# Optimization experiments

Hardware: AMD Instinct MI355X
Metric: run time of the kernel (lower is better)

## Reference

```python
import jax, jax.numpy as jnp
import numpy as np

H, W = 48, 48
L = H * W            # 2304 tokens
D = 256              # d_model
NH = 8               # heads (self and memory attn)
FF = 1024            # dim_feedforward
T = 2                # memory frames
BS = 1
GN_GROUPS = 32       # GNActDWConv2d default groups


def layernorm(x, g, b, eps=1e-5):
    m = jnp.mean(x, -1, keepdims=True)
    v = jnp.mean((x - m) ** 2, -1, keepdims=True)
    return (x - m) * jax.lax.rsqrt(v + eps) * g + b


def linear(x, Wt, b):
    # torch nn.Linear convention: Wt is [out, in]
    return x @ Wt.T + b


def mha_core(Q, K, V, nhead):
    # Q [Lq, bs, C], K/V [Lk, bs, C]; AOT MultiheadAttention core (eval: no dropout)
    Lq, bs, C = Q.shape
    hd = C // nhead
    Qh = (Q / np.float32(np.sqrt(hd))).reshape(Lq, bs, nhead, hd).transpose(1, 2, 0, 3)
    Kh = K.reshape(-1, bs, nhead, hd).transpose(1, 2, 0, 3)
    Vh = V.reshape(-1, bs, nhead, hd).transpose(1, 2, 0, 3)
    attn = jax.nn.softmax(jnp.einsum('bhqd,bhkd->bhqk', Qh, Kh), axis=-1)
    out = jnp.einsum('bhqk,bhkd->bhqd', attn, Vh)
    return out.transpose(2, 0, 1, 3).reshape(Lq, bs, C)


def groupnorm(x, g, b, groups, eps=1e-5):
    bs, c, h, w = x.shape
    xg = x.reshape(bs, groups, c // groups, h, w)
    m = jnp.mean(xg, (2, 3, 4), keepdims=True)
    v = jnp.mean((xg - m) ** 2, (2, 3, 4), keepdims=True)
    xg = (xg - m) * jax.lax.rsqrt(v + eps)
    return xg.reshape(bs, c, h, w) * g[None, :, None, None] + b[None, :, None, None]


def dwconv5(x, k):
    # depthwise 5x5, padding=2; x [bs,c,h,w], k [c,1,5,5]
    return jax.lax.conv_general_dilated(x, k, (1, 1), ((2, 2), (2, 2)),
                                        feature_group_count=x.shape[1])


def setup_inputs() -> dict:
    key = jax.random.key(0)
    ks = jax.random.split(key, 16)
    rn = lambda i, shape, s=1.0: jax.random.normal(ks[i], shape, jnp.float32) * s
    w = 0.02
    inp = {
        'tgt': rn(0, (L, BS, D)),
        'global_K': rn(1, (T, L, BS, D)),
        'global_V': rn(2, (T, L, BS, D)),
        'local_K': rn(3, (L, BS, D)),
        'local_V': rn(4, (L, BS, D)),
        # LayerNorms
        'ln1_g': jnp.ones(D, jnp.float32), 'ln1_b': jnp.zeros(D, jnp.float32),
        'ln2_g': jnp.ones(D, jnp.float32), 'ln2_b': jnp.zeros(D, jnp.float32),
        'ln3_g': jnp.ones(D, jnp.float32), 'ln3_b': jnp.zeros(D, jnp.float32),
        'ln4_g': jnp.ones(D, jnp.float32), 'ln4_b': jnp.zeros(D, jnp.float32),
        # self_attn (use_linear=True) Q/K/V + projection
        'sa_Wq': rn(5, (D, D), w), 'sa_bq': jnp.zeros(D, jnp.float32),
        'sa_Wk': rn(6, (D, D), w), 'sa_bk': jnp.zeros(D, jnp.float32),
        'sa_Wv': rn(7, (D, D), w), 'sa_bv': jnp.zeros(D, jnp.float32),
        'sa_Wo': rn(8, (D, D), w), 'sa_bo': jnp.zeros(D, jnp.float32),
        # block linear_Q
        'Wq': rn(9, (D, D), w), 'bq': jnp.zeros(D, jnp.float32),
        # long/short term attn projections (use_linear=False)
        'lt_Wo': rn(10, (D, D), w), 'lt_bo': jnp.zeros(D, jnp.float32),
        'st_Wo': rn(11, (D, D), w), 'st_bo': jnp.zeros(D, jnp.float32),
        # FFN: linear1 -> GN+GELU+DWConv -> linear2
        'W1': rn(12, (FF, D), w), 'b1': jnp.zeros(FF, jnp.float32),
        'gn_g': jnp.ones(FF, jnp.float32), 'gn_b': jnp.zeros(FF, jnp.float32),
        'dw_k': rn(13, (FF, 1, 5, 5), 0.05),
        'W2': rn(14, (D, FF), w), 'b2': jnp.zeros(D, jnp.float32),
    }
    return inp


def reference(tgt, global_K, global_V, local_K, local_V,
              ln1_g, ln1_b, ln2_g, ln2_b, ln3_g, ln3_b, ln4_g, ln4_b,
              sa_Wq, sa_bq, sa_Wk, sa_bk, sa_Wv, sa_bv, sa_Wo, sa_bo,
              Wq, bq, lt_Wo, lt_bo, st_Wo, st_bo,
              W1, b1, gn_g, gn_b, dw_k, W2, b2):
    # --- stage 1: self-attention ---
    _tgt = layernorm(tgt, ln1_g, ln1_b)
    q = linear(_tgt, sa_Wq, sa_bq)
    k = linear(_tgt, sa_Wk, sa_bk)
    v = linear(_tgt, sa_Wv, sa_bv)
    tgt2 = linear(mha_core(q, k, v, NH), sa_Wo, sa_bo)
    tgt = tgt + tgt2  # droppath is identity at eval

    # --- stage 2: long-term + short-term memory cross-attention ---
    _tgt = layernorm(tgt, ln2_g, ln2_b)
    curr_Q = linear(_tgt, Wq, bq)
    curr_K = curr_Q
    curr_V = _tgt

    flat_K = global_K.reshape(-1, BS, D)  # [T*L, bs, D]
    flat_V = global_V.reshape(-1, BS, D)
    tgt2 = linear(mha_core(curr_Q, flat_K, flat_V, NH), lt_Wo, lt_bo)

    k_st = layernorm(local_K + curr_K, ln4_g, ln4_b)
    v_st = layernorm(local_V + curr_V, ln4_g, ln4_b)
    tgt3 = linear(mha_core(curr_Q, k_st, v_st, NH), st_Wo, st_bo)

    tgt = tgt + tgt2 + tgt3

    # --- stage 3: FFN with GN + GELU + depthwise conv ---
    _tgt = layernorm(tgt, ln3_g, ln3_b)
    x = linear(_tgt, W1, b1)                        # [L, bs, FF]
    x = x.reshape(H, W, BS, FF).transpose(2, 3, 0, 1)  # [bs, FF, H, W]
    x = jax.nn.gelu(groupnorm(x, gn_g, gn_b, GN_GROUPS), approximate=False)
    x = dwconv5(x, dw_k)
    x = x.reshape(BS, FF, L).transpose(2, 0, 1)     # [L, bs, FF]
    tgt2 = linear(x, W2, b2)
    return tgt + tgt2
```

## Files before the change

kernel.cpp:

```cpp
#include <hip/hip_runtime.h>
#include <hip/hip_bf16.h>

#define L   2304
#define D   256
#define NHD 8
#define HD  32
#define FF  1024
#define HH  48
#define WWW 48
#define SPL 4
#define RCH 24
#define RP  (L / RCH)
#define S2LOG 0.25503486f

typedef unsigned short bfraw;
typedef __attribute__((ext_vector_type(8))) short s8v;
typedef __attribute__((ext_vector_type(4))) float f4v;

__device__ __forceinline__ bfraw f2b(float x) {
    __hip_bfloat16 h = __float2bfloat16(x);
    return __builtin_bit_cast(bfraw, h);
}

__global__ __launch_bounds__(256) void diag_kernel(float* __restrict__ out, float c, int n)
{
    int i = blockIdx.x * 256 + threadIdx.x;
    if (i < n) out[i] = c;
}

__global__ __launch_bounds__(256) void ln_kernel(
    const float* __restrict__ inA, const float* __restrict__ inB,
    const float* __restrict__ g, const float* __restrict__ b,
    float* __restrict__ out, bfraw* __restrict__ outb)
{
    int row = blockIdx.x, t = threadIdx.x;
    size_t idx = (size_t)row * D + t;
    float v = inA[idx];
    if (inB) v += inB[idx];
    __shared__ float rs[256], rq[256];
    rs[t] = v; rq[t] = v * v;
    __syncthreads();
    for (int o = 128; o > 0; o >>= 1) {
        if (t < o) { rs[t] += rs[t + o]; rq[t] += rq[t + o]; }
        __syncthreads();
    }
    float mean = rs[0] * (1.f / D);
    float var  = rq[0] * (1.f / D) - mean * mean;
    float rstd = rsqrtf(var + 1e-5f);
    float r = (v - mean) * rstd * g[t] + b[t];
    if (out)  out[idx]  = r;
    if (outb) outb[idx] = f2b(r);
}

__global__ __launch_bounds__(256) void ln2_ln4v(
    const float* __restrict__ t5, const float* __restrict__ lV,
    const float* __restrict__ g2, const float* __restrict__ b2,
    const float* __restrict__ g4, const float* __restrict__ b4,
    bfraw* __restrict__ out2b, float* __restrict__ outv)
{
    int row = blockIdx.x, t = threadIdx.x;
    size_t idx = (size_t)row * D + t;
    float v = t5[idx];
    __shared__ float rs[256], rq[256];
    rs[t] = v; rq[t] = v * v;
    __syncthreads();
    for (int o = 128; o > 0; o >>= 1) {
        if (t < o) { rs[t] += rs[t + o]; rq[t] += rq[t + o]; }
        __syncthreads();
    }
    float mean = rs[0] * (1.f / D);
    float var  = rq[0] * (1.f / D) - mean * mean;
    float rstd = rsqrtf(var + 1e-5f);
    float r2 = (v - mean) * rstd * g2[t] + b2[t];
    out2b[idx] = f2b(r2);
    float u = r2 + lV[idx];
    __syncthreads();
    rs[t] = u; rq[t] = u * u;
    __syncthreads();
    for (int o = 128; o > 0; o >>= 1) {
        if (t < o) { rs[t] += rs[t + o]; rq[t] += rq[t + o]; }
        __syncthreads();
    }
    float mean2 = rs[0] * (1.f / D);
    float var2  = rq[0] * (1.f / D) - mean2 * mean2;
    float rstd2 = rsqrtf(var2 + 1e-5f);
    outv[idx] = (u - mean2) * rstd2 * g4[t] + b4[t];
}

__global__ __launch_bounds__(256) void ln_cvtT(
    const float* __restrict__ t1, const float* __restrict__ lK,
    const float* __restrict__ g4, const float* __restrict__ b4,
    bfraw* __restrict__ kb2,
    const float* __restrict__ vsrc, bfraw* __restrict__ vtb2)
{
    __shared__ float rs[256], rq[256];
    __shared__ float Ls[32][33];
    int t = threadIdx.x;
    if (blockIdx.x < L) {
        int row = blockIdx.x;
        size_t idx = (size_t)row * D + t;
        float v = t1[idx] + lK[idx];
        rs[t] = v; rq[t] = v * v;
        __syncthreads();
        for (int o = 128; o > 0; o >>= 1) {
            if (t < o) { rs[t] += rs[t + o]; rq[t] += rq[t + o]; }
            __syncthreads();
        }
        float mean = rs[0] * (1.f / D);
        float var  = rq[0] * (1.f / D) - mean * mean;
        float rstd = rsqrtf(var + 1e-5f);
        kb2[idx] = f2b((v - mean) * rstd * g4[t] + b4[t]);
    } else {
        int idx = blockIdx.x - L;
        int n0 = (idx >> 3) * 32, h = idx & 7;
        int nl = t >> 3, dq = t & 7;
        float4 v = *reinterpret_cast<const float4*>(vsrc + (size_t)(n0 + nl) * D + h * HD + dq * 4);
        Ls[nl][dq*4+0] = v.x; Ls[nl][dq*4+1] = v.y;
        Ls[nl][dq*4+2] = v.z; Ls[nl][dq*4+3] = v.w;
        __syncthreads();
        int dl = t >> 3, nq = t & 7;
        ushort4 o;
        o.x = f2b(Ls[nq*4+0][dl]); o.y = f2b(Ls[nq*4+1][dl]);
        o.z = f2b(Ls[nq*4+2][dl]); o.w = f2b(Ls[nq*4+3][dl]);
        *reinterpret_cast<ushort4*>(vtb2 + (size_t)(h * HD + dl) * L + n0 + nq * 4) = o;
    }
}

__global__ __launch_bounds__(256) void gemm_mfma(
    const bfraw* __restrict__ A, const float* __restrict__ W,
    const float* __restrict__ bias, const float* res, float* out,
    bfraw* __restrict__ outb, float oscale,
    int M, int N, int K)
{
    __shared__ __attribute__((aligned(16))) short Wl[64][32];
    int t = threadIdx.x;
    int w = t >> 6, l = t & 63;
    int lo = l & 15, quad = l >> 4;
    int m0 = blockIdx.x * 32, n0 = blockIdx.y * 64;
    int wr = (w & 1) * 16, wc = (w >> 1) * 32;
    f4v acc[2];
    acc[0] = (f4v){0.f, 0.f, 0.f, 0.f};
    acc[1] = (f4v){0.f, 0.f, 0.f, 0.f};

    int aswz = (quad ^ ((lo >> 2) & 3)) * 8;
    int srow = t >> 3, spart = t & 7;
    const bfraw* ap = A + (size_t)(m0 + wr + lo) * K + quad * 8;

    for (int k0 = 0; k0 < K; k0 += 32) {
        float4 w4[2];
        #pragma unroll
        for (int i = 0; i < 2; i++)
            w4[i] = *reinterpret_cast<const float4*>(W + (size_t)(n0 + i * 32 + srow) * K + k0 + spart * 4);
        s8v af = *reinterpret_cast<const s8v*>(ap + k0);
        __syncthreads();
        #pragma unroll
        for (int i = 0; i < 2; i++) {
            int row = i * 32 + srow;
            int col = ((spart >> 1) ^ ((row >> 2) & 3)) * 8 + (spart & 1) * 4;
            ushort4 wb;
            wb.x = f2b(w4[i].x); wb.y = f2b(w4[i].y); wb.z = f2b(w4[i].z); wb.w = f2b(w4[i].w);
            *reinterpret_cast<ushort4*>(&Wl[row][col]) = wb;
        }
        __syncthreads();
        #pragma unroll
        for (int j = 0; j < 2; j++) {
            int rw = wc + j * 16 + lo;
            s8v wf = *reinterpret_cast<const s8v*>(&Wl[rw][aswz]);
            acc[j] = __builtin_amdgcn_mfma_f32_16x16x32_bf16(af, wf, acc[j], 0, 0, 0);
        }
    }

    #pragma unroll
    for (int j = 0; j < 2; j++) {
        #pragma unroll
        for (int r = 0; r < 4; r++) {
            int mrow = m0 + wr + quad * 4 + r;
            int ncol = n0 + wc + j * 16 + lo;
            float v = acc[j][r] + bias[ncol];
            size_t idx = (size_t)mrow * N + ncol;
            if (res) v += res[idx];
            if (out) out[idx] = v;
            if (outb) outb[idx] = f2b(v * oscale);
        }
    }
}

__global__ __launch_bounds__(256) void gemm_dual(
    const bfraw* __restrict__ A1, const float* __restrict__ W1, const float* __restrict__ b1,
    const bfraw* __restrict__ A2, const float* __restrict__ W2, const float* __restrict__ b2,
    const float* __restrict__ res, float* __restrict__ out)
{
    __shared__ __attribute__((aligned(16))) short Wl[64][32];
    int t = threadIdx.x;
    int w = t >> 6, l = t & 63;
    int lo = l & 15, quad = l >> 4;
    int m0 = blockIdx.x * 32, n0 = blockIdx.y * 64;
    int wr = (w & 1) * 16, wc = (w >> 1) * 32;
    f4v acc[2];
    acc[0] = (f4v){0.f, 0.f, 0.f, 0.f};
    acc[1] = (f4v){0.f, 0.f, 0.f, 0.f};

    int aswz = (quad ^ ((lo >> 2) & 3)) * 8;
    int srow = t >> 3, spart = t & 7;

    #pragma unroll
    for (int half = 0; half < 2; half++) {
        const bfraw* ap = (half ? A2 : A1) + (size_t)(m0 + wr + lo) * D + quad * 8;
        const float* W  = half ? W2 : W1;
        for (int k0 = 0; k0 < D; k0 += 32) {
            float4 w4[2];
            #pragma unroll
            for (int i = 0; i < 2; i++)
                w4[i] = *reinterpret_cast<const float4*>(W + (size_t)(n0 + i * 32 + srow) * D + k0 + spart * 4);
            s8v af = *reinterpret_cast<const s8v*>(ap + k0);
            __syncthreads();
            #pragma unroll
            for (int i = 0; i < 2; i++) {
                int row = i * 32 + srow;
                int col = ((spart >> 1) ^ ((row >> 2) & 3)) * 8 + (spart & 1) * 4;
                ushort4 wb;
                wb.x = f2b(w4[i].x); wb.y = f2b(w4[i].y); wb.z = f2b(w4[i].z); wb.w = f2b(w4[i].w);
                *reinterpret_cast<ushort4*>(&Wl[row][col]) = wb;
            }
            __syncthreads();
            #pragma unroll
            for (int j = 0; j < 2; j++) {
                int rw = wc + j * 16 + lo;
                s8v wf = *reinterpret_cast<const s8v*>(&Wl[rw][aswz]);
                acc[j] = __builtin_amdgcn_mfma_f32_16x16x32_bf16(af, wf, acc[j], 0, 0, 0);
            }
        }
    }

    #pragma unroll
    for (int j = 0; j < 2; j++) {
        #pragma unroll
        for (int r = 0; r < 4; r++) {
            int mrow = m0 + wr + quad * 4 + r;
            int ncol = n0 + wc + j * 16 + lo;
            size_t idx = (size_t)mrow * D + ncol;
            out[idx] = acc[j][r] + b1[ncol] + b2[ncol] + res[idx];
        }
    }
}

__global__ __launch_bounds__(256) void gemm_qkv(
    const bfraw* __restrict__ A,
    const float* __restrict__ Wq_, const float* __restrict__ bq_,
    const float* __restrict__ Wk_, const float* __restrict__ bk_,
    const float* __restrict__ Wv_, const float* __restrict__ bv_,
    bfraw* __restrict__ qb, bfraw* __restrict__ kb, bfraw* __restrict__ vtb)
{
    __shared__ __attribute__((aligned(16))) short Wl[64][32];
    int t = threadIdx.x;
    int w = t >> 6, l = t & 63;
    int lo = l & 15, quad = l >> 4;
    int sel = blockIdx.y >> 2;
    int m0 = blockIdx.x * 32, n0 = (blockIdx.y & 3) * 64;
    int wr = (w & 1) * 16, wc = (w >> 1) * 32;
    const float* W    = (sel == 0) ? Wq_ : (sel == 1) ? Wk_ : Wv_;
    const float* bias = (sel == 0) ? bq_ : (sel == 1) ? bk_ : bv_;
    f4v acc[2];
    acc[0] = (f4v){0.f, 0.f, 0.f, 0.f};
    acc[1] = (f4v){0.f, 0.f, 0.f, 0.f};

    int aswz = (quad ^ ((lo >> 2) & 3)) * 8;
    int srow = t >> 3, spart = t & 7;
    const bfraw* ap = A + (size_t)(m0 + wr + lo) * D + quad * 8;

    for (int k0 = 0; k0 < D; k0 += 32) {
        float4 w4[2];
        #pragma unroll
        for (int i = 0; i < 2; i++)
            w4[i] = *reinterpret_cast<const float4*>(W + (size_t)(n0 + i * 32 + srow) * D + k0 + spart * 4);
        s8v af = *reinterpret_cast<const s8v*>(ap + k0);
        __syncthreads();
        #pragma unroll
        for (int i = 0; i < 2; i++) {
            int row = i * 32 + srow;
            int col = ((spart >> 1) ^ ((row >> 2) & 3)) * 8 + (spart & 1) * 4;
            ushort4 wb;
            wb.x = f2b(w4[i].x); wb.y = f2b(w4[i].y); wb.z = f2b(w4[i].z); wb.w = f2b(w4[i].w);
            *reinterpret_cast<ushort4*>(&Wl[row][col]) = wb;
        }
        __syncthreads();
        #pragma unroll
        for (int j = 0; j < 2; j++) {
            int rw = wc + j * 16 + lo;
            s8v wf = *reinterpret_cast<const s8v*>(&Wl[rw][aswz]);
            acc[j] = __builtin_amdgcn_mfma_f32_16x16x32_bf16(af, wf, acc[j], 0, 0, 0);
        }
    }

    #pragma unroll
    for (int j = 0; j < 2; j++) {
        #pragma unroll
        for (int r = 0; r < 4; r++) {
            int mrow = m0 + wr + quad * 4 + r;
            int ncol = n0 + wc + j * 16 + lo;
            float v = acc[j][r] + bias[ncol];
            if (sel == 0)      qb[(size_t)mrow * D + ncol] = f2b(v * S2LOG);
            else if (sel == 1) kb[(size_t)mrow * D + ncol] = f2b(v);
            else               vtb[(size_t)ncol * L + mrow] = f2b(v);
        }
    }
}

__global__ __launch_bounds__(256) void cvt_both(
    const float* __restrict__ gK, bfraw* __restrict__ kb1,
    const float* __restrict__ gV, bfraw* __restrict__ vtb1)
{
    __shared__ float Ls[32][33];
    int t = threadIdx.x;
    if (blockIdx.y < NHD) {
        int h = blockIdx.y, n0 = blockIdx.x * 32;
        const int N = 2 * L;
        int nl = t >> 3, dq = t & 7;
        float4 v = *reinterpret_cast<const float4*>(gV + (size_t)(n0 + nl) * D + h * HD + dq * 4);
        Ls[nl][dq*4+0] = v.x; Ls[nl][dq*4+1] = v.y;
        Ls[nl][dq*4+2] = v.z; Ls[nl][dq*4+3] = v.w;
        __syncthreads();
        int dl = t >> 3, nq = t & 7;
        ushort4 o;
        o.x = f2b(Ls[nq*4+0][dl]); o.y = f2b(Ls[nq*4+1][dl]);
        o.z = f2b(Ls[nq*4+2][dl]); o.w = f2b(Ls[nq*4+3][dl]);
        *reinterpret_cast<ushort4*>(vtb1 + (size_t)(h * HD + dl) * N + n0 + nq * 4) = o;
    } else {
        size_t i = ((size_t)(blockIdx.x * 8 + (blockIdx.y - NHD)) * 256 + t) * 4;
        float4 v = *reinterpret_cast<const float4*>(gK + i);
        ushort4 o;
        o.x = f2b(v.x); o.y = f2b(v.y); o.z = f2b(v.z); o.w = f2b(v.w);
        *reinterpret_cast<ushort4*>(kb1 + i) = o;
    }
}

__device__ __forceinline__ void attn_core(
    const bfraw* __restrict__ Qb, const bfraw* __restrict__ Kb,
    const bfraw* __restrict__ Vt, float* __restrict__ OP,
    float* __restrict__ ML, int Lk, int chunk, int zz,
    short (*Ks)[32], short (*Vts)[72], short (*Ps)[72], float (*Tb)[33])
{
    int t = threadIdx.x;
    int w = t >> 6, l = t & 63;
    int h = blockIdx.y, q0 = blockIdx.x * 64 + w * 16;
    int lo = l & 15, quad = l >> 4;
    int kb = zz * chunk, ke = kb + chunk;

    s8v qf = *reinterpret_cast<const s8v*>(Qb + (size_t)(q0 + lo) * D + h * HD + quad * 8);
    int kswz = (quad ^ ((lo >> 2) & 3)) * 8;

    int skey = t >> 2, spart = t & 3;
    int kcol = (spart ^ ((skey >> 2) & 3)) * 8;
    int sd = t >> 3, svp = t & 7;
    const bfraw* kp = Kb + (size_t)skey * D + h * HD + spart * 8;
    const bfraw* vp = Vt + (size_t)(h * HD + sd) * Lk + svp * 8;

    float l_r = 0.f;
    f4v o0 = {0.f, 0.f, 0.f, 0.f}, o1 = {0.f, 0.f, 0.f, 0.f};

    for (int k0 = kb; k0 < ke; k0 += 64) {
        s8v kv = *reinterpret_cast<const s8v*>(kp + (size_t)k0 * D);
        s8v vv = *reinterpret_cast<const s8v*>(vp + k0);
        __syncthreads();
        *reinterpret_cast<s8v*>(&Ks[skey][kcol]) = kv;
        *reinterpret_cast<s8v*>(&Vts[sd][svp * 8]) = vv;
        __syncthreads();

        f4v sc4[4];
        #pragma unroll
        for (int s = 0; s < 4; s++) {
            s8v kf = *reinterpret_cast<const s8v*>(&Ks[lo + 16 * s][kswz]);
            sc4[s] = __builtin_amdgcn_mfma_f32_16x16x32_bf16(kf, qf, (f4v){0.f,0.f,0.f,0.f}, 0, 0, 0);
        }
        float ls = 0.f;
        #pragma unroll
        for (int s = 0; s < 4; s++) {
            float p0 = __builtin_amdgcn_exp2f(sc4[s][0]);
            float p1 = __builtin_amdgcn_exp2f(sc4[s][1]);
            float p2 = __builtin_amdgcn_exp2f(sc4[s][2]);
            float p3 = __builtin_amdgcn_exp2f(sc4[s][3]);
            ls += p0 + p1 + p2 + p3;
            ushort4 pk;
            pk.x = f2b(p0); pk.y = f2b(p1); pk.z = f2b(p2); pk.w = f2b(p3);
            *reinterpret_cast<ushort4*>(&Ps[lo][s * 16 + quad * 4]) = pk;
        }
        ls += __shfl_xor(ls, 16);
        ls += __shfl_xor(ls, 32);
        l_r += ls;
        #pragma unroll
        for (int kc = 0; kc < 2; kc++) {
            s8v pf = *reinterpret_cast<const s8v*>(&Ps[lo][kc * 32 + quad * 8]);
            s8v v0 = *reinterpret_cast<const s8v*>(&Vts[lo][kc * 32 + quad * 8]);
            s8v v1 = *reinterpret_cast<const s8v*>(&Vts[16 + lo][kc * 32 + quad * 8]);
            o0 = __builtin_amdgcn_mfma_f32_16x16x32_bf16(v0, pf, o0, 0, 0, 0);
            o1 = __builtin_amdgcn_mfma_f32_16x16x32_bf16(v1, pf, o1, 0, 0, 0);
        }
    }

    #pragma unroll
    for (int r = 0; r < 4; r++) {
        Tb[lo][quad * 4 + r]      = o0[r];
        Tb[lo][16 + quad * 4 + r] = o1[r];
    }
    float* Oz = OP + (size_t)zz * L * D;
    int ql = l >> 2, dq = (l & 3) * 8;
    float4 u0, u1;
    u0.x = Tb[ql][dq + 0]; u0.y = Tb[ql][dq + 1];
    u0.z = Tb[ql][dq + 2]; u0.w = Tb[ql][dq + 3];
    u1.x = Tb[ql][dq + 4]; u1.y = Tb[ql][dq + 5];
    u1.z = Tb[ql][dq + 6]; u1.w = Tb[ql][dq + 7];
    *reinterpret_cast<float4*>(Oz + (size_t)(q0 + ql) * D + h * HD + dq)     = u0;
    *reinterpret_cast<float4*>(Oz + (size_t)(q0 + ql) * D + h * HD + dq + 4) = u1;
    if (l < 16)
        ML[((size_t)zz * NHD + h) * L + q0 + lo] = l_r;
}

__global__ __launch_bounds__(256) void attn_mfma_split(
    const bfraw* __restrict__ Qb, const bfraw* __restrict__ Kb,
    const bfraw* __restrict__ Vt, float* __restrict__ OP,
    float* __restrict__ ML, int Lk, int chunk)
{
    __shared__ __attribute__((aligned(16))) short Ks[64][32];
    __shared__ __attribute__((aligned(16))) short Vts[32][72];
    __shared__ __attribute__((aligned(16))) short Ps[4][16][72];
    __shared__ float Tb[4][16][33];
    int w = threadIdx.x >> 6;
    attn_core(Qb, Kb, Vt, OP, ML, Lk, chunk, blockIdx.z, Ks, Vts, Ps[w], Tb[w]);
}

__global__ __launch_bounds__(256) void attn_ltst(
    const bfraw* __restrict__ Qb,
    const bfraw* __restrict__ K_lt, const bfraw* __restrict__ V_lt,
    float* __restrict__ OP_lt, float* __restrict__ ML_lt,
    const bfraw* __restrict__ K_st, const bfraw* __restrict__ V_st,
    float* __restrict__ OP_st, float* __restrict__ ML_st)
{
    __shared__ __attribute__((aligned(16))) short Ks[64][32];
    __shared__ __attribute__((aligned(16))) short Vts[32][72];
    __shared__ __attribute__((aligned(16))) short Ps[4][16][72];
    __shared__ float Tb[4][16][33];
    int w = threadIdx.x >> 6;
    int z = blockIdx.z;
    if (z < 2)
        attn_core(Qb, K_lt, V_lt, OP_lt, ML_lt, 2 * L, L, z, Ks, Vts, Ps[w], Tb[w]);
    else
        attn_core(Qb, K_st, V_st, OP_st, ML_st, L, L / 2, z - 2, Ks, Vts, Ps[w], Tb[w]);
}

__global__ __launch_bounds__(256) void attn_combine(
    const float* __restrict__ OP, const float* __restrict__ ML,
    bfraw* __restrict__ Ob)
{
    int q = blockIdx.x, t = threadIdx.x, h = t >> 5;
    float wl = 0.f, acc = 0.f;
    #pragma unroll
    for (int s = 0; s < SPL; s++) {
        wl  += ML[((size_t)s * NHD + h) * L + q];
        acc += OP[(size_t)s * L * D + (size_t)q * D + t];
    }
    Ob[(size_t)q * D + t] = f2b(acc / wl);
}

__global__ __launch_bounds__(256) void combine2_both(
    const float* __restrict__ OP_lt, const float* __restrict__ ML_lt, bfraw* __restrict__ Ob_lt,
    const float* __restrict__ OP_st, const float* __restrict__ ML_st, bfraw* __restrict__ Ob_st)
{
    int q = blockIdx.x, t = threadIdx.x, h = t >> 5;
    const float* OP = blockIdx.y ? OP_st : OP_lt;
    const float* ML = blockIdx.y ? ML_st : ML_lt;
    bfraw* Ob = blockIdx.y ? Ob_st : Ob_lt;
    float wl = 0.f, acc = 0.f;
    #pragma unroll
    for (int s = 0; s < 2; s++) {
        wl  += ML[((size_t)s * NHD + h) * L + q];
        acc += OP[(size_t)s * L * D + (size_t)q * D + t];
    }
    Ob[(size_t)q * D + t] = f2b(acc / wl);
}

__global__ __launch_bounds__(256) void gn_stats_part(
    const float* __restrict__ X, float* __restrict__ ps)
{
    int g = blockIdx.x, rc = blockIdx.y, t = threadIdx.x;
    int cq = (t & 7) * 4;
    int rl = t >> 3;
    int r0 = rc * RP;
    float s = 0.f, sq = 0.f;
    #pragma unroll
    for (int p = 0; p < RP / 32; p++) {
        int l = r0 + p * 32 + rl;
        float4 v = *reinterpret_cast<const float4*>(X + (size_t)l * FF + g * 32 + cq);
        s  += v.x + v.y + v.z + v.w;
        sq += v.x*v.x + v.y*v.y + v.z*v.z + v.w*v.w;
    }
    __shared__ float rs[256], rq[256];
    rs[t] = s; rq[t] = sq;
    __syncthreads();
    for (int o = 128; o > 0; o >>= 1) {
        if (t < o) { rs[t] += rs[t + o]; rq[t] += rq[t + o]; }
        __syncthreads();
    }
    if (t == 0) {
        ps[(g * RCH + rc) * 2]     = rs[0];
        ps[(g * RCH + rc) * 2 + 1] = rq[0];
    }
}

__global__ __launch_bounds__(256) void gn_gelu_dwconv(
    const float* __restrict__ X, const float* __restrict__ ps,
    const float* __restrict__ gg, const float* __restrict__ gb,
    const float* __restrict__ Kw, bfraw* __restrict__ Y)
{
    __shared__ float tile[144][64];
    int h0 = blockIdx.x * 8, w0 = blockIdx.y * 8, c0 = blockIdx.z * 64;
    int t = threadIdx.x;
    int c = t & 63;
    int cg = (c0 + c) >> 5;
    float s = 0.f, sq = 0.f;
    #pragma unroll
    for (int i = 0; i < RCH; i++) {
        s  += ps[(cg * RCH + i) * 2];
        sq += ps[(cg * RCH + i) * 2 + 1];
    }
    float n = (float)(L * 32);
    float mu = s / n;
    float rs = rsqrtf(sq / n - mu * mu + 1e-5f);
    float ga = gg[c0 + c], be = gb[c0 + c];

    for (int i = t; i < 144 * 64; i += 256) {
        int sp = i >> 6;
        int hy = h0 + (sp / 12) - 2, wx = w0 + (sp % 12) - 2;
        float v = 0.f;
        if (hy >= 0 && hy < HH && wx >= 0 && wx < WWW) {
            float x = X[(size_t)(hy * WWW + wx) * FF + c0 + c];
            x = (x - mu) * rs * ga + be;
            v = 0.5f * x * (1.f + erff(x * 0.70710678118654752f));
        }
        tile[sp][c] = v;
    }
    float kw[25];
    #pragma unroll
    for (int i = 0; i < 25; i++) kw[i] = Kw[(size_t)(c0 + c) * 25 + i];
    __syncthreads();

    int sgrp = t >> 6;
    for (int sIdx = 0; sIdx < 16; sIdx++) {
        int sp = sgrp * 16 + sIdx;
        int oh = sp >> 3, ow = sp & 7;
        float acc = 0.f;
        #pragma unroll
        for (int ky = 0; ky < 5; ky++)
            #pragma unroll
            for (int kx = 0; kx < 5; kx++)
                acc += tile[(oh + ky) * 12 + ow + kx][c] * kw[ky * 5 + kx];
        Y[(size_t)((h0 + oh) * WWW + w0 + ow) * FF + c0 + c] = f2b(acc);
    }
}

extern "C" void kernel_launch(void* const* d_in, const int* in_sizes, int n_in,
                              void* d_out, int out_size, void* d_ws, size_t ws_size,
                              hipStream_t stream)
{
    (void)in_sizes;
    float* out = (float*)d_out;

    if (n_in != 34) {
        diag_kernel<<<(out_size + 255) / 256, 256, 0, stream>>>(out, 2000.f, out_size);
        return;
    }

    const float* tgt    = (const float*)d_in[0];
    const float* gK     = (const float*)d_in[1];
    const float* gV     = (const float*)d_in[2];
    const float* lK     = (const float*)d_in[3];
    const float* lV     = (const float*)d_in[4];
    const float* ln1_g  = (const float*)d_in[5];
    const float* ln1_b  = (const float*)d_in[6];
    const float* ln2_g  = (const float*)d_in[7];
    const float* ln2_b  = (const float*)d_in[8];
    const float* ln3_g  = (const float*)d_in[9];
    const float* ln3_b  = (const float*)d_in[10];
    const float* ln4_g  = (const float*)d_in[11];
    const float* ln4_b  = (const float*)d_in[12];
    const float* sa_Wq  = (const float*)d_in[13];
    const float* sa_bq  = (const float*)d_in[14];
    const float* sa_Wk  = (const float*)d_in[15];
    const float* sa_bk  = (const float*)d_in[16];
    const float* sa_Wv  = (const float*)d_in[17];
    const float* sa_bv  = (const float*)d_in[18];
    const float* sa_Wo  = (const float*)d_in[19];
    const float* sa_bo  = (const float*)d_in[20];
    const float* Wq     = (const float*)d_in[21];
    const float* bq     = (const float*)d_in[22];
    const float* lt_Wo  = (const float*)d_in[23];
    const float* lt_bo  = (const float*)d_in[24];
    const float* st_Wo  = (const float*)d_in[25];
    const float* st_bo  = (const float*)d_in[26];
    const float* W1w    = (const float*)d_in[27];
    const float* b1w    = (const float*)d_in[28];
    const float* gn_g   = (const float*)d_in[29];
    const float* gn_b   = (const float*)d_in[30];
    const float* dw_k   = (const float*)d_in[31];
    const float* W2w    = (const float*)d_in[32];
    const float* b2w    = (const float*)d_in[33];

    const size_t LD = (size_t)L * D;
    const size_t NEED = (6 * LD + (size_t)L * FF + 64) * 4;
    float* ws = (float*)d_ws;
    float* t0 = ws + 0 * LD;
    float* t1 = ws + 1 * LD;
    float* t2 = ws + 2 * LD;
    float* t3 = ws + 3 * LD;
    float* t4 = ws + 4 * LD;
    float* t5 = ws + 5 * LD;
    float* X1 = t0;
    float* X2 = ws + 6 * LD;
    bfraw* qb   = (bfraw*)X2;
    bfraw* kb1  = qb + LD;
    bfraw* vtb1 = qb + 3 * LD;
    bfraw* kb2  = qb + 5 * LD;
    bfraw* vtb2 = qb + 6 * LD;
    float* OP   = ws;
    float* OPlt = t0;
    float* OPst = t2;
    float* ML   = X2 + (7 * LD) / 2;
    float* MLlt = ML;
    float* MLst = ML + 2 * (size_t)NHD * L;
    float* PS   = ML;
    bfraw* t0b  = (bfraw*)t0;
    bfraw* t3b  = (bfraw*)t3;
    bfraw* t4b  = (bfraw*)t4;
    bfraw* obLT = t4b;
    bfraw* obST = t4b + LD;
    bfraw* X2b  = (bfraw*)X2;

    if (ws_size < NEED) {
        int wsMiB = (int)(ws_size >> 20); if (wsMiB > 63) wsMiB = 63;
        diag_kernel<<<(out_size + 255) / 256, 256, 0, stream>>>(out, 64.f + (float)wsMiB, out_size);
        return;
    }

    dim3 gDD(L / 32, D / 64);
    dim3 gDF(L / 32, FF / 64);
    dim3 gQKV(L / 32, 12);
    dim3 gATS(L / 64, NHD, SPL);
    dim3 gAT2(L / 64, NHD, 4);
    dim3 gCB(2 * L / 32, NHD + 8);
    dim3 gC2(L, 2);
    dim3 gGN(32, RCH);
    dim3 gDW(6, 6, 16);

    ln_kernel<<<L, 256, 0, stream>>>(tgt, nullptr, ln1_g, ln1_b, nullptr, t0b);
    gemm_qkv<<<gQKV, 256, 0, stream>>>(t0b, sa_Wq, sa_bq, sa_Wk, sa_bk, sa_Wv, sa_bv,
                                       qb, kb2, vtb2);
    attn_mfma_split<<<gATS, 256, 0, stream>>>(qb, kb2, vtb2, OP, ML, L, L / SPL);
    attn_combine<<<L, 256, 0, stream>>>(OP, ML, t4b);
    gemm_mfma<<<gDD, 256, 0, stream>>>(t4b, sa_Wo, sa_bo, tgt, t5, nullptr, 1.f, L, D, D);

    ln2_ln4v<<<L, 256, 0, stream>>>(t5, lV, ln2_g, ln2_b, ln4_g, ln4_b, t3b, t0);
    gemm_mfma<<<gDD, 256, 0, stream>>>(t3b, Wq, bq, nullptr, t1, qb, S2LOG, L, D, D);
    ln_cvtT<<<L + (L / 32) * NHD, 256, 0, stream>>>(t1, lK, ln4_g, ln4_b, kb2, t0, vtb2);
    cvt_both<<<gCB, 256, 0, stream>>>(gK, kb1, gV, vtb1);
    attn_ltst<<<gAT2, 256, 0, stream>>>(qb, kb1, vtb1, OPlt, MLlt, kb2, vtb2, OPst, MLst);
    combine2_both<<<gC2, 256, 0, stream>>>(OPlt, MLlt, obLT, OPst, MLst, obST);
    gemm_dual<<<gDD, 256, 0, stream>>>(obLT, lt_Wo, lt_bo, obST, st_Wo, st_bo, t5, t5);

    ln_kernel<<<L, 256, 0, stream>>>(t5, nullptr, ln3_g, ln3_b, nullptr, t4b);
    gemm_mfma<<<gDF, 256, 0, stream>>>(t4b, W1w, b1w, nullptr, X1, nullptr, 1.f, L, FF, D);
    gn_stats_part<<<gGN, 256, 0, stream>>>(X1, PS);
    gn_gelu_dwconv<<<gDW, 256, 0, stream>>>(X1, PS, gn_g, gn_b, dw_k, X2b);
    gemm_mfma<<<gDD, 256, 0, stream>>>(X2b, W2w, b2w, t5, out, nullptr, 1.f, L, D, FF);
}
```

Measured before the change: 311.5 us.

## Fuse GN stats into W1 GEMM epilogue and merge memory cvt into LN2

Removes the separate GroupNorm partial-stats kernel: the FFN W1 GEMM epilogue now reduces per-wave sums and sums of squares via shuffles and atomically accumulates them per group into PS, which the LN3 kernel zeroes beforehand. The global K/V bf16 conversion kernel is merged into the LN2/LN4v kernel as extra blocks. This cuts two launches and a full re-read of the FFN activation, at the cost of float atomics (non-deterministic summation order) and an extra epilogue reduction in every GEMM call.

```diff
diff --git a/kernel.cpp b/kernel.cpp
--- a/kernel.cpp
+++ b/kernel.cpp
@@ -9,8 +9,6 @@
 #define HH  48
 #define WWW 48
 #define SPL 4
-#define RCH 24
-#define RP  (L / RCH)
 #define S2LOG 0.25503486f
 
 typedef unsigned short bfraw;
@@ -31,9 +29,11 @@
 __global__ __launch_bounds__(256) void ln_kernel(
     const float* __restrict__ inA, const float* __restrict__ inB,
     const float* __restrict__ g, const float* __restrict__ b,
-    float* __restrict__ out, bfraw* __restrict__ outb)
+    float* __restrict__ out, bfraw* __restrict__ outb,
+    float* __restrict__ zps)
 {
     int row = blockIdx.x, t = threadIdx.x;
+    if (zps && row == 0 && t < 64) zps[t] = 0.f;
     size_t idx = (size_t)row * D + t;
     float v = inA[idx];
     if (inB) v += inB[idx];
@@ -52,39 +52,68 @@
     if (outb) outb[idx] = f2b(r);
 }
 
-__global__ __launch_bounds__(256) void ln2_ln4v(
+__global__ __launch_bounds__(256) void ln2cvt(
     const float* __restrict__ t5, const float* __restrict__ lV,
     const float* __restrict__ g2, const float* __restrict__ b2,
     const float* __restrict__ g4, const float* __restrict__ b4,
-    bfraw* __restrict__ out2b, float* __restrict__ outv)
-{
-    int row = blockIdx.x, t = threadIdx.x;
-    size_t idx = (size_t)row * D + t;
-    float v = t5[idx];
+    bfraw* __restrict__ out2b, float* __restrict__ outv,
+    const float* __restrict__ gK, bfraw* __restrict__ kb1,
+    const float* __restrict__ gV, bfraw* __restrict__ vtb1)
+{
     __shared__ float rs[256], rq[256];
-    rs[t] = v; rq[t] = v * v;
-    __syncthreads();
-    for (int o = 128; o > 0; o >>= 1) {
-        if (t < o) { rs[t] += rs[t + o]; rq[t] += rq[t + o]; }
-        __syncthreads();
-    }
-    float mean = rs[0] * (1.f / D);
-    float var  = rq[0] * (1.f / D) - mean * mean;
-    float rstd = rsqrtf(var + 1e-5f);
-    float r2 = (v - mean) * rstd * g2[t] + b2[t];
-    out2b[idx] = f2b(r2);
-    float u = r2 + lV[idx];
-    __syncthreads();
-    rs[t] = u; rq[t] = u * u;
-    __syncthreads();
-    for (int o = 128; o > 0; o >>= 1) {
-        if (t < o) { rs[t] += rs[t + o]; rq[t] += rq[t + o]; }
-        __syncthreads();
-    }
-    float mean2 = rs[0] * (1.f / D);
-    float var2  = rq[0] * (1.f / D) - mean2 * mean2;
-    float rstd2 = rsqrtf(var2 + 1e-5f);
-    outv[idx] = (u - mean2) * rstd2 * g4[t] + b4[t];
+    __shared__ float Ls[32][33];
+    int t = threadIdx.x;
+    if (blockIdx.x < L) {
+        int row = blockIdx.x;
+        size_t idx = (size_t)row * D + t;
+        float v = t5[idx];
+        rs[t] = v; rq[t] = v * v;
+        __syncthreads();
+        for (int o = 128; o > 0; o >>= 1) {
+            if (t < o) { rs[t] += rs[t + o]; rq[t] += rq[t + o]; }
+            __syncthreads();
+        }
+        float mean = rs[0] * (1.f / D);
+        float var  = rq[0] * (1.f / D) - mean * mean;
+        float rstd = rsqrtf(var + 1e-5f);
+        float r2 = (v - mean) * rstd * g2[t] + b2[t];
+        out2b[idx] = f2b(r2);
+        float u = r2 + lV[idx];
+        __syncthreads();
+        rs[t] = u; rq[t] = u * u;
+        __syncthreads();
+        for (int o = 128; o > 0; o >>= 1) {
+            if (t < o) { rs[t] += rs[t + o]; rq[t] += rq[t + o]; }
+            __syncthreads();
+        }
+        float mean2 = rs[0] * (1.f / D);
+        float var2  = rq[0] * (1.f / D) - mean2 * mean2;
+        float rstd2 = rsqrtf(var2 + 1e-5f);
+        outv[idx] = (u - mean2) * rstd2 * g4[t] + b4[t];
+    } else {
+        int idx = blockIdx.x - L;
+        int ix = idx % (2 * L / 32), iy = idx / (2 * L / 32);
+        if (iy < NHD) {
+            int h = iy, n0 = ix * 32;
+            const int N = 2 * L;
+            int nl = t >> 3, dq = t & 7;
+            float4 v = *reinterpret_cast<const float4*>(gV + (size_t)(n0 + nl) * D + h * HD + dq * 4);
+            Ls[nl][dq*4+0] = v.x; Ls[nl][dq*4+1] = v.y;
+            Ls[nl][dq*4+2] = v.z; Ls[nl][dq*4+3] = v.w;
+            __syncthreads();
+            int dl = t >> 3, nq = t & 7;
+            ushort4 o;
+            o.x = f2b(Ls[nq*4+0][dl]); o.y = f2b(Ls[nq*4+1][dl]);
+            o.z = f2b(Ls[nq*4+2][dl]); o.w = f2b(Ls[nq*4+3][dl]);
+            *reinterpret_cast<ushort4*>(vtb1 + (size_t)(h * HD + dl) * N + n0 + nq * 4) = o;
+        } else {
+            size_t i = ((size_t)(ix * 8 + (iy - NHD)) * 256 + t) * 4;
+            float4 v = *reinterpret_cast<const float4*>(gK + i);
+            ushort4 o;
+            o.x = f2b(v.x); o.y = f2b(v.y); o.z = f2b(v.z); o.w = f2b(v.w);
+            *reinterpret_cast<ushort4*>(kb1 + i) = o;
+        }
+    }
 }
 
 __global__ __launch_bounds__(256) void ln_cvtT(
@@ -129,7 +158,7 @@
 __global__ __launch_bounds__(256) void gemm_mfma(
     const bfraw* __restrict__ A, const float* __restrict__ W,
     const float* __restrict__ bias, const float* res, float* out,
-    bfraw* __restrict__ outb, float oscale,
+    bfraw* __restrict__ outb, float oscale, float* __restrict__ ps,
     int M, int N, int K)
 {
     __shared__ __attribute__((aligned(16))) short Wl[64][32];
@@ -170,6 +199,7 @@
         }
     }
 
+    float sl = 0.f, sq = 0.f;
     #pragma unroll
     for (int j = 0; j < 2; j++) {
         #pragma unroll
@@ -181,6 +211,19 @@
             if (res) v += res[idx];
             if (out) out[idx] = v;
             if (outb) outb[idx] = f2b(v * oscale);
+            sl += v; sq += v * v;
+        }
+    }
+    if (ps) {
+        #pragma unroll
+        for (int off = 1; off < 64; off <<= 1) {
+            sl += __shfl_xor(sl, off);
+            sq += __shfl_xor(sq, off);
+        }
+        if (l == 0) {
+            int g = (n0 + wc) >> 5;
+            atomicAdd(&ps[g * 2],     sl);
+            atomicAdd(&ps[g * 2 + 1], sq);
         }
     }
 }
@@ -306,34 +349,6 @@
     }
 }
 
-__global__ __launch_bounds__(256) void cvt_both(
-    const float* __restrict__ gK, bfraw* __restrict__ kb1,
-    const float* __restrict__ gV, bfraw* __restrict__ vtb1)
-{
-    __shared__ float Ls[32][33];
-    int t = threadIdx.x;
-    if (blockIdx.y < NHD) {
-        int h = blockIdx.y, n0 = blockIdx.x * 32;
-        const int N = 2 * L;
-        int nl = t >> 3, dq = t & 7;
-        float4 v = *reinterpret_cast<const float4*>(gV + (size_t)(n0 + nl) * D + h * HD + dq * 4);
-        Ls[nl][dq*4+0] = v.x; Ls[nl][dq*4+1] = v.y;
-        Ls[nl][dq*4+2] = v.z; Ls[nl][dq*4+3] = v.w;
-        __syncthreads();
-        int dl = t >> 3, nq = t & 7;
-        ushort4 o;
-        o.x = f2b(Ls[nq*4+0][dl]); o.y = f2b(Ls[nq*4+1][dl]);
-        o.z = f2b(Ls[nq*4+2][dl]); o.w = f2b(Ls[nq*4+3][dl]);
-        *reinterpret_cast<ushort4*>(vtb1 + (size_t)(h * HD + dl) * N + n0 + nq * 4) = o;
-    } else {
-        size_t i = ((size_t)(blockIdx.x * 8 + (blockIdx.y - NHD)) * 256 + t) * 4;
-        float4 v = *reinterpret_cast<const float4*>(gK + i);
-        ushort4 o;
-        o.x = f2b(v.x); o.y = f2b(v.y); o.z = f2b(v.z); o.w = f2b(v.w);
-        *reinterpret_cast<ushort4*>(kb1 + i) = o;
-    }
-}
-
 __device__ __forceinline__ void attn_core(
     const bfraw* __restrict__ Qb, const bfraw* __restrict__ Kb,
     const bfraw* __restrict__ Vt, float* __restrict__ OP,
@@ -478,34 +493,6 @@
     Ob[(size_t)q * D + t] = f2b(acc / wl);
 }
 
-__global__ __launch_bounds__(256) void gn_stats_part(
-    const float* __restrict__ X, float* __restrict__ ps)
-{
-    int g = blockIdx.x, rc = blockIdx.y, t = threadIdx.x;
-    int cq = (t & 7) * 4;
-    int rl = t >> 3;
-    int r0 = rc * RP;
-    float s = 0.f, sq = 0.f;
-    #pragma unroll
-    for (int p = 0; p < RP / 32; p++) {
-        int l = r0 + p * 32 + rl;
-        float4 v = *reinterpret_cast<const float4*>(X + (size_t)l * FF + g * 32 + cq);
-        s  += v.x + v.y + v.z + v.w;
-        sq += v.x*v.x + v.y*v.y + v.z*v.z + v.w*v.w;
-    }
-    __shared__ float rs[256], rq[256];
-    rs[t] = s; rq[t] = sq;
-    __syncthreads();
-    for (int o = 128; o > 0; o >>= 1) {
-        if (t < o) { rs[t] += rs[t + o]; rq[t] += rq[t + o]; }
-        __syncthreads();
-    }
-    if (t == 0) {
-        ps[(g * RCH + rc) * 2]     = rs[0];
-        ps[(g * RCH + rc) * 2 + 1] = rq[0];
-    }
-}
-
 __global__ __launch_bounds__(256) void gn_gelu_dwconv(
     const float* __restrict__ X, const float* __restrict__ ps,
     const float* __restrict__ gg, const float* __restrict__ gb,
@@ -516,15 +503,9 @@
     int t = threadIdx.x;
     int c = t & 63;
     int cg = (c0 + c) >> 5;
-    float s = 0.f, sq = 0.f;
-    #pragma unroll
-    for (int i = 0; i < RCH; i++) {
-        s  += ps[(cg * RCH + i) * 2];
-        sq += ps[(cg * RCH + i) * 2 + 1];
-    }
     float n = (float)(L * 32);
-    float mu = s / n;
-    float rs = rsqrtf(sq / n - mu * mu + 1e-5f);
+    float mu = ps[cg * 2] / n;
+    float rs = rsqrtf(ps[cg * 2 + 1] / n - mu * mu + 1e-5f);
     float ga = gg[c0 + c], be = gb[c0 + c];
 
     for (int i = t; i < 144 * 64; i += 256) {
@@ -645,29 +626,28 @@
     dim3 gQKV(L / 32, 12);
     dim3 gATS(L / 64, NHD, SPL);
     dim3 gAT2(L / 64, NHD, 4);
-    dim3 gCB(2 * L / 32, NHD + 8);
     dim3 gC2(L, 2);
-    dim3 gGN(32, RCH);
     dim3 gDW(6, 6, 16);
-
-    ln_kernel<<<L, 256, 0, stream>>>(tgt, nullptr, ln1_g, ln1_b, nullptr, t0b);
+    int  gLN2 = L + (2 * L / 32) * (NHD + 8) / (2 * L / 32) * 0;
+    (void)gLN2;
+
+    ln_kernel<<<L, 256, 0, stream>>>(tgt, nullptr, ln1_g, ln1_b, nullptr, t0b, nullptr);
     gemm_qkv<<<gQKV, 256, 0, stream>>>(t0b, sa_Wq, sa_bq, sa_Wk, sa_bk, sa_Wv, sa_bv,
                                        qb, kb2, vtb2);
     attn_mfma_split<<<gATS, 256, 0, stream>>>(qb, kb2, vtb2, OP, ML, L, L / SPL);
     attn_combine<<<L, 256, 0, stream>>>(OP, ML, t4b);
-    gemm_mfma<<<gDD, 256, 0, stream>>>(t4b, sa_Wo, sa_bo, tgt, t5, nullptr, 1.f, L, D, D);
-
-    ln2_ln4v<<<L, 256, 0, stream>>>(t5, lV, ln2_g, ln2_b, ln4_g, ln4_b, t3b, t0);
-    gemm_mfma<<<gDD, 256, 0, stream>>>(t3b, Wq, bq, nullptr, t1, qb, S2LOG, L, D, D);
+    gemm_mfma<<<gDD, 256, 0, stream>>>(t4b, sa_Wo, sa_bo, tgt, t5, nullptr, 1.f, nullptr, L, D, D);
+
+    ln2cvt<<<L + (2 * L / 32) * (NHD + 8), 256, 0, stream>>>(
+        t5, lV, ln2_g, ln2_b, ln4_g, ln4_b, t3b, t0, gK, kb1, gV, vtb1);
+    gemm_mfma<<<gDD, 256, 0, stream>>>(t3b, Wq, bq, nullptr, t1, qb, S2LOG, nullptr, L, D, D);
     ln_cvtT<<<L + (L / 32) * NHD, 256, 0, stream>>>(t1, lK, ln4_g, ln4_b, kb2, t0, vtb2);
-    cvt_both<<<gCB, 256, 0, stream>>>(gK, kb1, gV, vtb1);
     attn_ltst<<<gAT2, 256, 0, stream>>>(qb, kb1, vtb1, OPlt, MLlt, kb2, vtb2, OPst, MLst);
     combine2_both<<<gC2, 256, 0, stream>>>(OPlt, MLlt, obLT, OPst, MLst, obST);
     gemm_dual<<<gDD, 256, 0, stream>>>(obLT, lt_Wo, lt_bo, obST, st_Wo, st_bo, t5, t5);
 
-    ln_kernel<<<L, 256, 0, stream>>>(t5, nullptr, ln3_g, ln3_b, nullptr, t4b);
-    gemm_mfma<<<gDF, 256, 0, stream>>>(t4b, W1w, b1w, nullptr, X1, nullptr, 1.f, L, FF, D);
-    gn_stats_part<<<gGN, 256, 0, stream>>>(X1, PS);
+    ln_kernel<<<L, 256, 0, stream>>>(t5, nullptr, ln3_g, ln3_b, nullptr, t4b, PS);
+    gemm_mfma<<<gDF, 256, 0, stream>>>(t4b, W1w, b1w, nullptr, X1, nullptr, 1.f, PS, L, FF, D);
     gn_gelu_dwconv<<<gDW, 256, 0, stream>>>(X1, PS, gn_g, gn_b, dw_k, X2b);
-    gemm_mfma<<<gDD, 256, 0, stream>>>(X2b, W2w, b2w, t5, out, nullptr, 1.f, L, D, FF);
-}
+    gemm_mfma<<<gDD, 256, 0, stream>>>(X2b, W2w, b2w, t5, out, nullptr, 1.f, nullptr, L, D, FF);
+}
```

New measurement: 363.3 us. +16.7%, slower.
